# Kernel tuning notes

Hardware: AMD Instinct MI355X
Metric: run time of the kernel (lower is better)

Reference implementation:

```python
import jax, jax.numpy as jnp
import numpy as np

B, NF, H = 1024, 64, 512


def setup_inputs() -> dict:
    key = jax.random.key(0)
    ks = jax.random.split(key, 12)
    sc_in2 = 1.0 / np.sqrt(2 * H)
    sc_in1 = 1.0 / np.sqrt(H)
    inp = {
        "field_vectors": jax.random.normal(ks[0], (B, NF, H), dtype=jnp.float32),
        # and_fusion: Linear(2H->H), ReLU, Linear(H->H)
        "and_W1": jax.random.uniform(ks[1], (2 * H, H), jnp.float32, -sc_in2, sc_in2),
        "and_b1": jax.random.uniform(ks[2], (H,), jnp.float32, -sc_in2, sc_in2),
        "and_W2": jax.random.uniform(ks[3], (H, H), jnp.float32, -sc_in1, sc_in1),
        "and_b2": jax.random.uniform(ks[4], (H,), jnp.float32, -sc_in1, sc_in1),
        # or_fusion: Linear(2H->H), ReLU, Linear(H->H)
        "or_W1": jax.random.uniform(ks[5], (2 * H, H), jnp.float32, -sc_in2, sc_in2),
        "or_b1": jax.random.uniform(ks[6], (H,), jnp.float32, -sc_in2, sc_in2),
        "or_W2": jax.random.uniform(ks[7], (H, H), jnp.float32, -sc_in1, sc_in1),
        "or_b2": jax.random.uniform(ks[8], (H,), jnp.float32, -sc_in1, sc_in1),
        # not_transform: Linear(H->H), Tanh
        "not_W": jax.random.uniform(ks[9], (H, H), jnp.float32, -sc_in1, sc_in1),
        "not_b": jax.random.uniform(ks[10], (H,), jnp.float32, -sc_in1, sc_in1),
        # Disjoint index structure so the torch skip-set logic is a no-op:
        # 'and' pairs use fields 0..31, 'or' pairs use 32..47, leftovers 48..63.
        "not_idx": 48 + jnp.arange(8, dtype=jnp.int32),
        "and_pairs": jnp.arange(32, dtype=jnp.int32).reshape(16, 2),
        "or_pairs": (32 + jnp.arange(16, dtype=jnp.int32)).reshape(8, 2),
        "leftover_idx": 48 + jnp.arange(16, dtype=jnp.int32),
    }
    return inp


def _mlp2(x, W1, b1, W2, b2):
    # Linear -> ReLU -> Linear
    return jax.nn.relu(x @ W1 + b1) @ W2 + b2


def reference(field_vectors, and_W1, and_b1, and_W2, and_b2,
              or_W1, or_b1, or_W2, or_b2, not_W, not_b,
              not_idx, and_pairs, or_pairs, leftover_idx):
    # In-place 'not' transform on selected fields (Tanh(Linear))
    fv = field_vectors.at[:, not_idx].set(
        jnp.tanh(field_vectors[:, not_idx] @ not_W + not_b))
    # Gather (i, j) pairs, concat along feature dim -> [B, P, 2H]
    cat_and = jnp.concatenate([fv[:, and_pairs[:, 0]], fv[:, and_pairs[:, 1]]], axis=-1)
    fused_and = _mlp2(cat_and, and_W1, and_b1, and_W2, and_b2)  # [B, 16, H]
    cat_or = jnp.concatenate([fv[:, or_pairs[:, 0]], fv[:, or_pairs[:, 1]]], axis=-1)
    fused_or = _mlp2(cat_or, or_W1, or_b1, or_W2, or_b2)  # [B, 8, H]
    # Stack order matches torch loop: and results, or results, untouched fields
    return jnp.concatenate([fused_and, fused_or, fv[:, leftover_idx]], axis=1)
```

## Files before the change

kernel.cpp:

```cpp
#include <hip/hip_runtime.h>
#include <hip/hip_bf16.h>
#include <math.h>

typedef __attribute__((ext_vector_type(8))) __bf16 bf16x8;
typedef __attribute__((ext_vector_type(4))) float f32x4;

__device__ __forceinline__ unsigned short f2bf(float f) {
    union { float f; unsigned u; } v; v.f = f;
    unsigned r = v.u + 0x7fffu + ((v.u >> 16) & 1u);
    return (unsigned short)(r >> 16);
}
__device__ __forceinline__ unsigned int pk(float a, float b) {
    union { float f; unsigned u; } x, y; x.f = a; y.f = b;
    unsigned ra = (x.u + 0x7fffu + ((x.u >> 16) & 1u)) >> 16;
    unsigned rb = (y.u + 0x7fffu + ((y.u >> 16) & 1u)) & 0xffff0000u;
    return ra | rb;
}

__device__ __forceinline__ void gl2lds16(const unsigned short* g, unsigned short* l) {
    __builtin_amdgcn_global_load_lds(
        (const __attribute__((address_space(1))) unsigned int*)(g),
        (__attribute__((address_space(3))) unsigned int*)(l), 16, 0, 0);
}

struct PrepArgs {
    const float* fv;
    unsigned short* fvb;
    const int *and_pairs, *or_pairs, *not_idx, *lidx;
    float* out;
    const float* W[5];
    unsigned short* WT[5];
    int N[5];
    int tstart[6];
};

__global__ __launch_bounds__(256) void prep_kernel(PrepArgs a) {
    __shared__ float tile[64][65];
    const int blk = blockIdx.x;
    const int tid = threadIdx.x;

    if (blk < 448) {
        int m = 0;
        while (blk >= a.tstart[m + 1]) m++;
        const float* src = a.W[m];
        unsigned short* dst = a.WT[m];
        const int N = a.N[m];
        const int t = blk - a.tstart[m];
        const int ntn = N >> 6;
        const int tk = t / ntn, tn = t % ntn;
        const int c = tid & 63, r0 = tid >> 6;
        #pragma unroll
        for (int r = r0; r < 64; r += 4)
            tile[r][c] = src[(size_t)(tk * 64 + r) * N + tn * 64 + c];
        __syncthreads();
        const int l = tid & 63;
        #pragma unroll
        for (int fi = tid >> 6; fi < 8; fi += 4) {
            const int ktl = fi & 1, cgl = fi >> 1;
            const int kt = tk * 2 + ktl, cg = tn * 4 + cgl;
            const int kb = ktl * 32 + (l >> 4) * 8;
            const int nb = cgl * 16 + (l & 15);
            uint4 o;
            o.x = pk(tile[kb + 0][nb], tile[kb + 1][nb]);
            o.y = pk(tile[kb + 2][nb], tile[kb + 3][nb]);
            o.z = pk(tile[kb + 4][nb], tile[kb + 5][nb]);
            o.w = pk(tile[kb + 6][nb], tile[kb + 7][nb]);
            ((uint4*)dst)[((size_t)kt * 32 + cg) * 64 + l] = o;
        }
        return;
    }

    const int t = (blk - 448) * 256 + tid;
    const int lane = tid & 63;
    const size_t e = (size_t)t * 8;
    const int c = (int)(e & 511);
    const int f = (int)((e >> 9) & 63);
    const int b = (int)(e >> 15);
    const float4 v0 = *(const float4*)(a.fv + e);
    const float4 v1 = *(const float4*)(a.fv + e + 4);
    const int am = (lane < 32) ? a.and_pairs[lane] : -1;
    const int om = (lane < 16) ? a.or_pairs[lane]  : -1;
    const int nm = (lane <  8) ? a.not_idx[lane]   : -1;
    const int lm = (lane < 16) ? a.lidx[lane]      : -1;
    const unsigned long long bn = __ballot(nm == f);
    const unsigned long long bu = __ballot(am == f) | __ballot(om == f) | bn;
    const unsigned long long bl = __ballot(lm == f);
    if (bu) {
        uint4 o;
        o.x = pk(v0.x, v0.y); o.y = pk(v0.z, v0.w);
        o.z = pk(v1.x, v1.y); o.w = pk(v1.z, v1.w);
        ((uint4*)a.fvb)[t] = o;
    }
    if (bl && !bn) {
        const int ls = (int)__builtin_ctzll(bl);
        float* d = a.out + ((size_t)b * 40 + 24 + ls) * 512 + c;
        *(float4*)(d)     = v0;
        *(float4*)(d + 4) = v1;
    }
}

#define LOADB(DST, WTP, K0)                                                  \
    _Pragma("unroll") for (int ni = 0; ni < 4; ni++)                         \
        DST[ni] = *(const bf16x8*)((WTP) +                                   \
            ((((size_t)(K0) >> 5) * 32 + cg0 + ni) << 9) + (lane << 3));

#define MMAC(BF, AF)                                                         \
    _Pragma("unroll") for (int mi = 0; mi < 4; mi++)                         \
    _Pragma("unroll") for (int ni = 0; ni < 4; ni++)                         \
        acc[mi][ni] = __builtin_amdgcn_mfma_f32_16x16x32_bf16(               \
            AF[mi], BF[ni], acc[mi][ni], 0, 0, 0);

template <int P, int K1, int SRCM, int PATH, int QBASE>
__device__ __forceinline__ void fused_seg(
    const unsigned short* __restrict__ A,
    const int* __restrict__ idx,
    const unsigned short* __restrict__ W1T,
    const float* __restrict__ b1,
    const unsigned short* __restrict__ W2T,
    const float* __restrict__ b2,
    float* __restrict__ out,
    const int* __restrict__ leftover,
    int local,
    unsigned short* As, unsigned short* hid) {

    const int tid  = threadIdx.x;
    const int lane = tid & 63, w = tid >> 6;
    const int ln15 = lane & 15;
    const int kq   = lane >> 4;
    const int wn   = w * 64;
    const int cg0  = w * 4;
    const int m0   = local * 64;

    const int skin = ((lane & 3) ^ ((lane >> 2) & 3)) * 8;
    const unsigned short *ar0, *ar1;
    {
        const int m = m0 + (w & 3) * 16 + (lane >> 2);
        if constexpr (SRCM == 0) {
            const int b = m / P, p = m % P;
            ar0 = A + ((size_t)b * 64 + idx[2 * p]) * 512;
            ar1 = A + ((size_t)b * 64 + idx[2 * p + 1]) * 512;
        } else {
            const int b = m >> 3, i = m & 7;
            ar0 = A + ((size_t)b * 64 + idx[i]) * 512;
            ar1 = ar0;
        }
    }
    auto stageA = [&](int buf, int t) {
        const int k0 = t * 32;
        const unsigned short* src;
        if constexpr (SRCM == 0)
            src = (k0 >= 512 ? ar1 + (k0 - 512) : ar0 + k0) + skin;
        else
            src = ar0 + k0 + skin;
        gl2lds16(src, &As[buf * 2048 + (w & 3) * 512]);
    };
    const int xsel = (kq ^ (lane & 3)) * 8;

    f32x4 acc[4][4];
    #pragma unroll
    for (int mi = 0; mi < 4; mi++)
        #pragma unroll
        for (int ni = 0; ni < 4; ni++)
            acc[mi][ni] = f32x4{0.f, 0.f, 0.f, 0.f};

    bf16x8 bA[4];

    constexpr int NT1 = K1 / 32;
    if (w < 4) { stageA(0, 0); stageA(1, 1); }
    __builtin_amdgcn_sched_barrier(0);

    for (int h = 0; h < NT1; h++) {
        asm volatile("s_waitcnt vmcnt(1) lgkmcnt(0)" ::: "memory");
        asm volatile("s_barrier" ::: "memory");
        LOADB(bA, W1T, h * 32);
        __builtin_amdgcn_sched_barrier(0);
        if (w < 4 && h + 2 < NT1) stageA((h + 2) & 3, h + 2);
        __builtin_amdgcn_sched_barrier(0);
        bf16x8 af[4];
        #pragma unroll
        for (int mi = 0; mi < 4; mi++)
            af[mi] = *(const bf16x8*)&As[(h & 3) * 2048 +
                                         (mi * 16 + ln15) * 32 + xsel];
        MMAC(bA, af);
        __builtin_amdgcn_sched_barrier(0);
    }

    if constexpr (PATH == 2) {
        int qmap[8];
        #pragma unroll
        for (int i = 0; i < 8; i++) {
            const int f = idx[i];
            int q = 24;
            for (int l = 0; l < 16; l++)
                if (leftover[l] == f) q = 24 + l;
            qmap[i] = q;
        }
        #pragma unroll
        for (int ni = 0; ni < 4; ni++) {
            const int n = wn + ni * 16 + ln15;
            const float bv = b1[n];
            #pragma unroll
            for (int mi = 0; mi < 4; mi++)
                #pragma unroll
                for (int j = 0; j < 4; j++) {
                    const int r = mi * 16 + kq * 4 + j;
                    const int m = m0 + r;
                    const int b = m >> 3, i = m & 7;
                    out[((size_t)b * 40 + qmap[i]) * 512 + n] =
                        tanhf(acc[mi][ni][j] + bv);
                }
        }
        return;
    }

    #pragma unroll
    for (int ni = 0; ni < 4; ni++) {
        const int n  = wn + ni * 16 + ln15;
        const float bv = b1[n];
        const int c8 = n >> 3;
        const int cl = (n & 7) * 2;
        #pragma unroll
        for (int mi = 0; mi < 4; mi++)
            #pragma unroll
            for (int j = 0; j < 4; j++) {
                const int r = mi * 16 + kq * 4 + j;
                float v = acc[mi][ni][j] + bv;
                v = v > 0.f ? v : 0.f;
                *(unsigned short*)((char*)hid + r * 1024 +
                                   ((c8 ^ (r & 7)) * 16) + cl) = f2bf(v);
            }
    }
    #pragma unroll
    for (int mi = 0; mi < 4; mi++)
        #pragma unroll
        for (int ni = 0; ni < 4; ni++)
            acc[mi][ni] = f32x4{0.f, 0.f, 0.f, 0.f};
    __syncthreads();

    for (int t2 = 0; t2 < 16; t2++) {
        LOADB(bA, W2T, t2 * 32);
        bf16x8 af[4];
        #pragma unroll
        for (int mi = 0; mi < 4; mi++) {
            const int r = mi * 16 + ln15;
            const int c8 = t2 * 4 + kq;
            af[mi] = *(const bf16x8*)((char*)hid + r * 1024 +
                                      ((c8 ^ (r & 7)) * 16));
        }
        MMAC(bA, af);
    }

    #pragma unroll
    for (int ni = 0; ni < 4; ni++) {
        const int n  = wn + ni * 16 + ln15;
        const float bv = b2[n];
        #pragma unroll
        for (int mi = 0; mi < 4; mi++)
            #pragma unroll
            for (int j = 0; j < 4; j++) {
                const int r = mi * 16 + kq * 4 + j;
                const int m = m0 + r;
                const int b = m / P, p = m % P;
                out[((size_t)b * 40 + QBASE + p) * 512 + n] =
                    acc[mi][ni][j] + bv;
            }
    }
}

struct FArgs {
    const unsigned short *fvb, *and_W1T, *and_W2T, *or_W1T, *or_W2T, *not_WT;
    const int *and_pairs, *or_pairs, *not_idx, *leftover;
    const float *and_b1, *and_b2, *or_b1, *or_b2, *not_b;
    float* out;
};

__global__ __launch_bounds__(512, 4) void fused_phase(FArgs a) {
    __shared__ __align__(16) unsigned short As[4 * 64 * 32];
    __shared__ __align__(16) unsigned short hid[64 * 512];
    const int blk = blockIdx.x;
    if (blk < 256)
        fused_seg<16, 1024, 0, 0, 0>(a.fvb, a.and_pairs, a.and_W1T, a.and_b1,
                                     a.and_W2T, a.and_b2, a.out, nullptr,
                                     blk, As, hid);
    else if (blk < 384)
        fused_seg<8, 1024, 0, 0, 16>(a.fvb, a.or_pairs, a.or_W1T, a.or_b1,
                                     a.or_W2T, a.or_b2, a.out, nullptr,
                                     blk - 256, As, hid);
    else
        fused_seg<8, 512, 1, 2, 24>(a.fvb, a.not_idx, a.not_WT, a.not_b,
                                    nullptr, nullptr, a.out, a.leftover,
                                    blk - 384, As, hid);
}

extern "C" void kernel_launch(void* const* d_in, const int* in_sizes, int n_in,
                              void* d_out, int out_size, void* d_ws, size_t ws_size,
                              hipStream_t stream) {
    const float* fv       = (const float*)d_in[0];
    const float* and_W1   = (const float*)d_in[1];
    const float* and_b1   = (const float*)d_in[2];
    const float* and_W2   = (const float*)d_in[3];
    const float* and_b2   = (const float*)d_in[4];
    const float* or_W1    = (const float*)d_in[5];
    const float* or_b1    = (const float*)d_in[6];
    const float* or_W2    = (const float*)d_in[7];
    const float* or_b2    = (const float*)d_in[8];
    const float* not_W    = (const float*)d_in[9];
    const float* not_b    = (const float*)d_in[10];
    const int* not_idx    = (const int*)d_in[11];
    const int* and_pairs  = (const int*)d_in[12];
    const int* or_pairs   = (const int*)d_in[13];
    const int* leftover   = (const int*)d_in[14];
    float* out = (float*)d_out;
    char* ws = (char*)d_ws;

    unsigned short* fvb     = (unsigned short*)(ws);
    unsigned short* and_W1T = (unsigned short*)(ws + 67108864);
    unsigned short* or_W1T  = (unsigned short*)(ws + 68157440);
    unsigned short* and_W2T = (unsigned short*)(ws + 69206016);
    unsigned short* or_W2T  = (unsigned short*)(ws + 69730304);
    unsigned short* not_WT  = (unsigned short*)(ws + 70254592);

    PrepArgs pa;
    pa.fv = fv; pa.fvb = fvb; pa.out = out;
    pa.and_pairs = and_pairs; pa.or_pairs = or_pairs;
    pa.not_idx = not_idx; pa.lidx = leftover;
    pa.W[0] = and_W1; pa.WT[0] = and_W1T; pa.N[0] = 512;
    pa.W[1] = or_W1;  pa.WT[1] = or_W1T;  pa.N[1] = 512;
    pa.W[2] = and_W2; pa.WT[2] = and_W2T; pa.N[2] = 512;
    pa.W[3] = or_W2;  pa.WT[3] = or_W2T;  pa.N[3] = 512;
    pa.W[4] = not_W;  pa.WT[4] = not_WT;  pa.N[4] = 512;
    pa.tstart[0] = 0;   pa.tstart[1] = 128; pa.tstart[2] = 256;
    pa.tstart[3] = 320; pa.tstart[4] = 384; pa.tstart[5] = 448;
    prep_kernel<<<dim3(448 + 16384), dim3(256), 0, stream>>>(pa);

    FArgs fa;
    fa.fvb = fvb;
    fa.and_W1T = and_W1T; fa.and_W2T = and_W2T;
    fa.or_W1T = or_W1T;   fa.or_W2T = or_W2T;   fa.not_WT = not_WT;
    fa.and_pairs = and_pairs; fa.or_pairs = or_pairs; fa.not_idx = not_idx;
    fa.leftover = leftover;
    fa.and_b1 = and_b1; fa.and_b2 = and_b2;
    fa.or_b1 = or_b1;   fa.or_b2 = or_b2;   fa.not_b = not_b;
    fa.out = out;
    fused_phase<<<dim3(512), dim3(512), 0, stream>>>(fa);
}
```

Baseline: 302.9 us.

## Scatter bf16 activations into pre-tiled swizzled A layouts during prep

The prep kernel now writes the bf16-converted field vectors straight into per-segment (and/or/not) A buffers, already gathered by pair and arranged in the tile order and XOR swizzle the GEMM consumes. The fused kernel then stages A with one contiguous global-to-LDS copy per tile and no per-row pair indirection. This removes the gather address computation and the scattered row reads in the GEMM's main loop, and makes its A loads fully contiguous. The cost is that the prep kernel's stores become scattered, and correctness relies on each field appearing in at most one and-pair and one or-pair slot (ctz picks a single match).

```diff
diff --git a/kernel.cpp b/kernel.cpp
--- a/kernel.cpp
+++ b/kernel.cpp
@@ -25,7 +25,7 @@
 
 struct PrepArgs {
     const float* fv;
-    unsigned short* fvb;
+    unsigned short *and_At, *or_At, *not_At;
     const int *and_pairs, *or_pairs, *not_idx, *lidx;
     float* out;
     const float* W[5];
@@ -82,14 +82,46 @@
     const int om = (lane < 16) ? a.or_pairs[lane]  : -1;
     const int nm = (lane <  8) ? a.not_idx[lane]   : -1;
     const int lm = (lane < 16) ? a.lidx[lane]      : -1;
+    const unsigned long long ba = __ballot(am == f);
+    const unsigned long long bo = __ballot(om == f);
     const unsigned long long bn = __ballot(nm == f);
-    const unsigned long long bu = __ballot(am == f) | __ballot(om == f) | bn;
     const unsigned long long bl = __ballot(lm == f);
-    if (bu) {
-        uint4 o;
-        o.x = pk(v0.x, v0.y); o.y = pk(v0.z, v0.w);
-        o.z = pk(v1.x, v1.y); o.w = pk(v1.z, v1.w);
-        ((uint4*)a.fvb)[t] = o;
+
+    uint4 o;
+    o.x = pk(v0.x, v0.y); o.y = pk(v0.z, v0.w);
+    o.z = pk(v1.x, v1.y); o.w = pk(v1.z, v1.w);
+    const int c8 = lane;
+    const int kc = c8 & 3;
+
+    if (ba) {
+        const int j = (int)__builtin_ctzll(ba);
+        const int m = b * 16 + (j >> 1);
+        const int kt = (j & 1) * 16 + (c8 >> 2);
+        const int r = m & 63;
+        const int l = ((r & 15) << 2) | (kc ^ (r & 3));
+        *(uint4*)(a.and_At +
+            (((((size_t)(m >> 6) * 32 + kt) << 2) | (unsigned)(r >> 4)) << 9) +
+            (l << 3)) = o;
+    }
+    if (bo) {
+        const int j = (int)__builtin_ctzll(bo);
+        const int m = b * 8 + (j >> 1);
+        const int kt = (j & 1) * 16 + (c8 >> 2);
+        const int r = m & 63;
+        const int l = ((r & 15) << 2) | (kc ^ (r & 3));
+        *(uint4*)(a.or_At +
+            (((((size_t)(m >> 6) * 32 + kt) << 2) | (unsigned)(r >> 4)) << 9) +
+            (l << 3)) = o;
+    }
+    if (bn) {
+        const int i = (int)__builtin_ctzll(bn);
+        const int m = b * 8 + i;
+        const int kt = c8 >> 2;
+        const int r = m & 63;
+        const int l = ((r & 15) << 2) | (kc ^ (r & 3));
+        *(uint4*)(a.not_At +
+            (((((size_t)(m >> 6) * 16 + kt) << 2) | (unsigned)(r >> 4)) << 9) +
+            (l << 3)) = o;
     }
     if (bl && !bn) {
         const int ls = (int)__builtin_ctzll(bl);
@@ -110,15 +142,15 @@
         acc[mi][ni] = __builtin_amdgcn_mfma_f32_16x16x32_bf16(               \
             AF[mi], BF[ni], acc[mi][ni], 0, 0, 0);
 
-template <int P, int K1, int SRCM, int PATH, int QBASE>
+template <int P, int K1, int PATH, int QBASE>
 __device__ __forceinline__ void fused_seg(
-    const unsigned short* __restrict__ A,
-    const int* __restrict__ idx,
+    const unsigned short* __restrict__ At,
     const unsigned short* __restrict__ W1T,
     const float* __restrict__ b1,
     const unsigned short* __restrict__ W2T,
     const float* __restrict__ b2,
     float* __restrict__ out,
+    const int* __restrict__ nidx,
     const int* __restrict__ leftover,
     int local,
     unsigned short* As, unsigned short* hid) {
@@ -130,29 +162,12 @@
     const int wn   = w * 64;
     const int cg0  = w * 4;
     const int m0   = local * 64;
-
-    const int skin = ((lane & 3) ^ ((lane >> 2) & 3)) * 8;
-    const unsigned short *ar0, *ar1;
-    {
-        const int m = m0 + (w & 3) * 16 + (lane >> 2);
-        if constexpr (SRCM == 0) {
-            const int b = m / P, p = m % P;
-            ar0 = A + ((size_t)b * 64 + idx[2 * p]) * 512;
-            ar1 = A + ((size_t)b * 64 + idx[2 * p + 1]) * 512;
-        } else {
-            const int b = m >> 3, i = m & 7;
-            ar0 = A + ((size_t)b * 64 + idx[i]) * 512;
-            ar1 = ar0;
-        }
-    }
+    constexpr int NTK = K1 / 32;
+
+    const unsigned short* abase =
+        At + (size_t)local * NTK * 2048 + ((w & 3) << 9) + (lane << 3);
     auto stageA = [&](int buf, int t) {
-        const int k0 = t * 32;
-        const unsigned short* src;
-        if constexpr (SRCM == 0)
-            src = (k0 >= 512 ? ar1 + (k0 - 512) : ar0 + k0) + skin;
-        else
-            src = ar0 + k0 + skin;
-        gl2lds16(src, &As[buf * 2048 + (w & 3) * 512]);
+        gl2lds16(abase + (size_t)t * 2048, &As[buf * 2048 + (w & 3) * 512]);
     };
     const int xsel = (kq ^ (lane & 3)) * 8;
 
@@ -165,16 +180,15 @@
 
     bf16x8 bA[4];
 
-    constexpr int NT1 = K1 / 32;
     if (w < 4) { stageA(0, 0); stageA(1, 1); }
     __builtin_amdgcn_sched_barrier(0);
 
-    for (int h = 0; h < NT1; h++) {
+    for (int h = 0; h < NTK; h++) {
         asm volatile("s_waitcnt vmcnt(1) lgkmcnt(0)" ::: "memory");
         asm volatile("s_barrier" ::: "memory");
         LOADB(bA, W1T, h * 32);
         __builtin_amdgcn_sched_barrier(0);
-        if (w < 4 && h + 2 < NT1) stageA((h + 2) & 3, h + 2);
+        if (w < 4 && h + 2 < NTK) stageA((h + 2) & 3, h + 2);
         __builtin_amdgcn_sched_barrier(0);
         bf16x8 af[4];
         #pragma unroll
@@ -189,7 +203,7 @@
         int qmap[8];
         #pragma unroll
         for (int i = 0; i < 8; i++) {
-            const int f = idx[i];
+            const int f = nidx[i];
             int q = 24;
             for (int l = 0; l < 16; l++)
                 if (leftover[l] == f) q = 24 + l;
@@ -268,8 +282,9 @@
 }
 
 struct FArgs {
-    const unsigned short *fvb, *and_W1T, *and_W2T, *or_W1T, *or_W2T, *not_WT;
-    const int *and_pairs, *or_pairs, *not_idx, *leftover;
+    const unsigned short *and_At, *or_At, *not_At;
+    const unsigned short *and_W1T, *and_W2T, *or_W1T, *or_W2T, *not_WT;
+    const int *not_idx, *leftover;
     const float *and_b1, *and_b2, *or_b1, *or_b2, *not_b;
     float* out;
 };
@@ -279,17 +294,17 @@
     __shared__ __align__(16) unsigned short hid[64 * 512];
     const int blk = blockIdx.x;
     if (blk < 256)
-        fused_seg<16, 1024, 0, 0, 0>(a.fvb, a.and_pairs, a.and_W1T, a.and_b1,
-                                     a.and_W2T, a.and_b2, a.out, nullptr,
-                                     blk, As, hid);
+        fused_seg<16, 1024, 0, 0>(a.and_At, a.and_W1T, a.and_b1,
+                                  a.and_W2T, a.and_b2, a.out,
+                                  nullptr, nullptr, blk, As, hid);
     else if (blk < 384)
-        fused_seg<8, 1024, 0, 0, 16>(a.fvb, a.or_pairs, a.or_W1T, a.or_b1,
-                                     a.or_W2T, a.or_b2, a.out, nullptr,
-                                     blk - 256, As, hid);
+        fused_seg<8, 1024, 0, 16>(a.or_At, a.or_W1T, a.or_b1,
+                                  a.or_W2T, a.or_b2, a.out,
+                                  nullptr, nullptr, blk - 256, As, hid);
     else
-        fused_seg<8, 512, 1, 2, 24>(a.fvb, a.not_idx, a.not_WT, a.not_b,
-                                    nullptr, nullptr, a.out, a.leftover,
-                                    blk - 384, As, hid);
+        fused_seg<8, 512, 2, 24>(a.not_At, a.not_WT, a.not_b,
+                                 nullptr, nullptr, a.out,
+                                 a.not_idx, a.leftover, blk - 384, As, hid);
 }
 
 extern "C" void kernel_launch(void* const* d_in, const int* in_sizes, int n_in,
@@ -313,15 +328,18 @@
     float* out = (float*)d_out;
     char* ws = (char*)d_ws;
 
-    unsigned short* fvb     = (unsigned short*)(ws);
-    unsigned short* and_W1T = (unsigned short*)(ws + 67108864);
-    unsigned short* or_W1T  = (unsigned short*)(ws + 68157440);
-    unsigned short* and_W2T = (unsigned short*)(ws + 69206016);
-    unsigned short* or_W2T  = (unsigned short*)(ws + 69730304);
-    unsigned short* not_WT  = (unsigned short*)(ws + 70254592);
+    unsigned short* and_At  = (unsigned short*)(ws);
+    unsigned short* or_At   = (unsigned short*)(ws + 33554432);
+    unsigned short* not_At  = (unsigned short*)(ws + 50331648);
+    unsigned short* and_W1T = (unsigned short*)(ws + 58720256);
+    unsigned short* or_W1T  = (unsigned short*)(ws + 59768832);
+    unsigned short* and_W2T = (unsigned short*)(ws + 60817408);
+    unsigned short* or_W2T  = (unsigned short*)(ws + 61341696);
+    unsigned short* not_WT  = (unsigned short*)(ws + 61865984);
 
     PrepArgs pa;
-    pa.fv = fv; pa.fvb = fvb; pa.out = out;
+    pa.fv = fv; pa.out = out;
+    pa.and_At = and_At; pa.or_At = or_At; pa.not_At = not_At;
     pa.and_pairs = and_pairs; pa.or_pairs = or_pairs;
     pa.not_idx = not_idx; pa.lidx = leftover;
     pa.W[0] = and_W1; pa.WT[0] = and_W1T; pa.N[0] = 512;
@@ -334,11 +352,10 @@
     prep_kernel<<<dim3(448 + 16384), dim3(256), 0, stream>>>(pa);
 
     FArgs fa;
-    fa.fvb = fvb;
+    fa.and_At = and_At; fa.or_At = or_At; fa.not_At = not_At;
     fa.and_W1T = and_W1T; fa.and_W2T = and_W2T;
     fa.or_W1T = or_W1T;   fa.or_W2T = or_W2T;   fa.not_WT = not_WT;
-    fa.and_pairs = and_pairs; fa.or_pairs = or_pairs; fa.not_idx = not_idx;
-    fa.leftover = leftover;
+    fa.not_idx = not_idx; fa.leftover = leftover;
     fa.and_b1 = and_b1; fa.and_b2 = and_b2;
     fa.or_b1 = or_b1;   fa.or_b2 = or_b2;   fa.not_b = not_b;
     fa.out = out;
```

After: 298.7 us. No clear change (-1.4%).

## Fuse fp32-to-bf16 conversion of activations into GEMM A-tile staging

Applied to the files above, without the earlier changes.

Drops the prep pass that converted the whole 128MB fp32 field tensor to a bf16 workspace. The fused GEMM kernel now loads fp32 rows directly through registers, converts them to bf16 and writes them to a double-buffered LDS tile, replacing the async global-to-LDS loads. The leftover-field copy moves into extra blocks of the fused kernel. This removes a full read and write of the activations, at the cost of register-staged loads with less latency hiding and twice the bytes per A tile.

```diff
diff --git a/kernel.cpp b/kernel.cpp
--- a/kernel.cpp
+++ b/kernel.cpp
@@ -17,85 +17,43 @@
     return ra | rb;
 }
 
-__device__ __forceinline__ void gl2lds16(const unsigned short* g, unsigned short* l) {
-    __builtin_amdgcn_global_load_lds(
-        (const __attribute__((address_space(1))) unsigned int*)(g),
-        (__attribute__((address_space(3))) unsigned int*)(l), 16, 0, 0);
-}
-
-struct PrepArgs {
-    const float* fv;
-    unsigned short* fvb;
-    const int *and_pairs, *or_pairs, *not_idx, *lidx;
-    float* out;
+struct WArgs {
     const float* W[5];
     unsigned short* WT[5];
     int N[5];
     int tstart[6];
 };
 
-__global__ __launch_bounds__(256) void prep_kernel(PrepArgs a) {
+__global__ __launch_bounds__(256) void wprep_kernel(WArgs a) {
     __shared__ float tile[64][65];
     const int blk = blockIdx.x;
     const int tid = threadIdx.x;
-
-    if (blk < 448) {
-        int m = 0;
-        while (blk >= a.tstart[m + 1]) m++;
-        const float* src = a.W[m];
-        unsigned short* dst = a.WT[m];
-        const int N = a.N[m];
-        const int t = blk - a.tstart[m];
-        const int ntn = N >> 6;
-        const int tk = t / ntn, tn = t % ntn;
-        const int c = tid & 63, r0 = tid >> 6;
-        #pragma unroll
-        for (int r = r0; r < 64; r += 4)
-            tile[r][c] = src[(size_t)(tk * 64 + r) * N + tn * 64 + c];
-        __syncthreads();
-        const int l = tid & 63;
-        #pragma unroll
-        for (int fi = tid >> 6; fi < 8; fi += 4) {
-            const int ktl = fi & 1, cgl = fi >> 1;
-            const int kt = tk * 2 + ktl, cg = tn * 4 + cgl;
-            const int kb = ktl * 32 + (l >> 4) * 8;
-            const int nb = cgl * 16 + (l & 15);
-            uint4 o;
-            o.x = pk(tile[kb + 0][nb], tile[kb + 1][nb]);
-            o.y = pk(tile[kb + 2][nb], tile[kb + 3][nb]);
-            o.z = pk(tile[kb + 4][nb], tile[kb + 5][nb]);
-            o.w = pk(tile[kb + 6][nb], tile[kb + 7][nb]);
-            ((uint4*)dst)[((size_t)kt * 32 + cg) * 64 + l] = o;
-        }
-        return;
-    }
-
-    const int t = (blk - 448) * 256 + tid;
-    const int lane = tid & 63;
-    const size_t e = (size_t)t * 8;
-    const int c = (int)(e & 511);
-    const int f = (int)((e >> 9) & 63);
-    const int b = (int)(e >> 15);
-    const float4 v0 = *(const float4*)(a.fv + e);
-    const float4 v1 = *(const float4*)(a.fv + e + 4);
-    const int am = (lane < 32) ? a.and_pairs[lane] : -1;
-    const int om = (lane < 16) ? a.or_pairs[lane]  : -1;
-    const int nm = (lane <  8) ? a.not_idx[lane]   : -1;
-    const int lm = (lane < 16) ? a.lidx[lane]      : -1;
-    const unsigned long long bn = __ballot(nm == f);
-    const unsigned long long bu = __ballot(am == f) | __ballot(om == f) | bn;
-    const unsigned long long bl = __ballot(lm == f);
-    if (bu) {
+    int m = 0;
+    while (blk >= a.tstart[m + 1]) m++;
+    const float* src = a.W[m];
+    unsigned short* dst = a.WT[m];
+    const int N = a.N[m];
+    const int t = blk - a.tstart[m];
+    const int ntn = N >> 6;
+    const int tk = t / ntn, tn = t % ntn;
+    const int c = tid & 63, r0 = tid >> 6;
+    #pragma unroll
+    for (int r = r0; r < 64; r += 4)
+        tile[r][c] = src[(size_t)(tk * 64 + r) * N + tn * 64 + c];
+    __syncthreads();
+    const int l = tid & 63;
+    #pragma unroll
+    for (int fi = tid >> 6; fi < 8; fi += 4) {
+        const int ktl = fi & 1, cgl = fi >> 1;
+        const int kt = tk * 2 + ktl, cg = tn * 4 + cgl;
+        const int kb = ktl * 32 + (l >> 4) * 8;
+        const int nb = cgl * 16 + (l & 15);
         uint4 o;
-        o.x = pk(v0.x, v0.y); o.y = pk(v0.z, v0.w);
-        o.z = pk(v1.x, v1.y); o.w = pk(v1.z, v1.w);
-        ((uint4*)a.fvb)[t] = o;
-    }
-    if (bl && !bn) {
-        const int ls = (int)__builtin_ctzll(bl);
-        float* d = a.out + ((size_t)b * 40 + 24 + ls) * 512 + c;
-        *(float4*)(d)     = v0;
-        *(float4*)(d + 4) = v1;
+        o.x = pk(tile[kb + 0][nb], tile[kb + 1][nb]);
+        o.y = pk(tile[kb + 2][nb], tile[kb + 3][nb]);
+        o.z = pk(tile[kb + 4][nb], tile[kb + 5][nb]);
+        o.w = pk(tile[kb + 6][nb], tile[kb + 7][nb]);
+        ((uint4*)dst)[((size_t)kt * 32 + cg) * 64 + l] = o;
     }
 }
 
@@ -110,9 +68,13 @@
         acc[mi][ni] = __builtin_amdgcn_mfma_f32_16x16x32_bf16(               \
             AF[mi], BF[ni], acc[mi][ni], 0, 0, 0);
 
-template <int P, int K1, int SRCM, int PATH, int QBASE>
+#define LBAR()                                                               \
+    asm volatile("s_waitcnt lgkmcnt(0)" ::: "memory");                       \
+    asm volatile("s_barrier" ::: "memory");
+
+template <int P, int K1, int PATH, int QBASE>
 __device__ __forceinline__ void fused_seg(
-    const unsigned short* __restrict__ A,
+    const float* __restrict__ fv,
     const int* __restrict__ idx,
     const unsigned short* __restrict__ W1T,
     const float* __restrict__ b1,
@@ -130,29 +92,35 @@
     const int wn   = w * 64;
     const int cg0  = w * 4;
     const int m0   = local * 64;
-
-    const int skin = ((lane & 3) ^ ((lane >> 2) & 3)) * 8;
-    const unsigned short *ar0, *ar1;
+    constexpr int NTK = K1 / 32;
+
+    const int r  = tid >> 3;
+    const int ks = tid & 7;
+    const float *ar0, *ar1;
     {
-        const int m = m0 + (w & 3) * 16 + (lane >> 2);
-        if constexpr (SRCM == 0) {
+        const int m = m0 + r;
+        if constexpr (PATH == 0) {
             const int b = m / P, p = m % P;
-            ar0 = A + ((size_t)b * 64 + idx[2 * p]) * 512;
-            ar1 = A + ((size_t)b * 64 + idx[2 * p + 1]) * 512;
+            ar0 = fv + ((size_t)b * 64 + idx[2 * p]) * 512 + ks * 4;
+            ar1 = fv + ((size_t)b * 64 + idx[2 * p + 1]) * 512 + ks * 4;
         } else {
             const int b = m >> 3, i = m & 7;
-            ar0 = A + ((size_t)b * 64 + idx[i]) * 512;
+            ar0 = fv + ((size_t)b * 64 + idx[i]) * 512 + ks * 4;
             ar1 = ar0;
         }
     }
-    auto stageA = [&](int buf, int t) {
+    auto ldA = [&](int t) -> float4 {
         const int k0 = t * 32;
-        const unsigned short* src;
-        if constexpr (SRCM == 0)
-            src = (k0 >= 512 ? ar1 + (k0 - 512) : ar0 + k0) + skin;
+        if constexpr (K1 == 1024)
+            return *(const float4*)(k0 >= 512 ? ar1 + (k0 - 512) : ar0 + k0);
         else
-            src = ar0 + k0 + skin;
-        gl2lds16(src, &As[buf * 2048 + (w & 3) * 512]);
+            return *(const float4*)(ar0 + k0);
+    };
+    unsigned short* const wdst =
+        As + r * 32 + (((ks >> 1) ^ (r & 3)) << 3) + ((ks & 1) << 2);
+    auto wrA = [&](int buf, float4 v) {
+        uint2 o; o.x = pk(v.x, v.y); o.y = pk(v.z, v.w);
+        *(uint2*)(wdst + buf * 2048) = o;
     };
     const int xsel = (kq ^ (lane & 3)) * 8;
 
@@ -165,24 +133,34 @@
 
     bf16x8 bA[4];
 
-    constexpr int NT1 = K1 / 32;
-    if (w < 4) { stageA(0, 0); stageA(1, 1); }
-    __builtin_amdgcn_sched_barrier(0);
-
-    for (int h = 0; h < NT1; h++) {
-        asm volatile("s_waitcnt vmcnt(1) lgkmcnt(0)" ::: "memory");
-        asm volatile("s_barrier" ::: "memory");
-        LOADB(bA, W1T, h * 32);
-        __builtin_amdgcn_sched_barrier(0);
-        if (w < 4 && h + 2 < NT1) stageA((h + 2) & 3, h + 2);
-        __builtin_amdgcn_sched_barrier(0);
-        bf16x8 af[4];
-        #pragma unroll
-        for (int mi = 0; mi < 4; mi++)
-            af[mi] = *(const bf16x8*)&As[(h & 3) * 2048 +
-                                         (mi * 16 + ln15) * 32 + xsel];
-        MMAC(bA, af);
-        __builtin_amdgcn_sched_barrier(0);
+    float4 va = ldA(0);
+    float4 vb = ldA(1);
+    wrA(0, va);
+    LBAR();
+
+    for (int h = 0; h < NTK; h += 2) {
+        {
+            LOADB(bA, W1T, h * 32);
+            if (h + 2 < NTK) va = ldA(h + 2);
+            bf16x8 af[4];
+            #pragma unroll
+            for (int mi = 0; mi < 4; mi++)
+                af[mi] = *(const bf16x8*)&As[(mi * 16 + ln15) * 32 + xsel];
+            MMAC(bA, af);
+            wrA(1, vb);
+            LBAR();
+        }
+        {
+            LOADB(bA, W1T, (h + 1) * 32);
+            if (h + 3 < NTK) vb = ldA(h + 3);
+            bf16x8 af[4];
+            #pragma unroll
+            for (int mi = 0; mi < 4; mi++)
+                af[mi] = *(const bf16x8*)&As[2048 + (mi * 16 + ln15) * 32 + xsel];
+            MMAC(bA, af);
+            if (h + 2 < NTK) { wrA(0, va); }
+            LBAR();
+        }
     }
 
     if constexpr (PATH == 2) {
@@ -203,8 +181,8 @@
             for (int mi = 0; mi < 4; mi++)
                 #pragma unroll
                 for (int j = 0; j < 4; j++) {
-                    const int r = mi * 16 + kq * 4 + j;
-                    const int m = m0 + r;
+                    const int rr = mi * 16 + kq * 4 + j;
+                    const int m = m0 + rr;
                     const int b = m >> 3, i = m & 7;
                     out[((size_t)b * 40 + qmap[i]) * 512 + n] =
                         tanhf(acc[mi][ni][j] + bv);
@@ -223,11 +201,11 @@
         for (int mi = 0; mi < 4; mi++)
             #pragma unroll
             for (int j = 0; j < 4; j++) {
-                const int r = mi * 16 + kq * 4 + j;
+                const int rr = mi * 16 + kq * 4 + j;
                 float v = acc[mi][ni][j] + bv;
                 v = v > 0.f ? v : 0.f;
-                *(unsigned short*)((char*)hid + r * 1024 +
-                                   ((c8 ^ (r & 7)) * 16) + cl) = f2bf(v);
+                *(unsigned short*)((char*)hid + rr * 1024 +
+                                   ((c8 ^ (rr & 7)) * 16) + cl) = f2bf(v);
             }
     }
     #pragma unroll
@@ -242,10 +220,10 @@
         bf16x8 af[4];
         #pragma unroll
         for (int mi = 0; mi < 4; mi++) {
-            const int r = mi * 16 + ln15;
+            const int rr = mi * 16 + ln15;
             const int c8 = t2 * 4 + kq;
-            af[mi] = *(const bf16x8*)((char*)hid + r * 1024 +
-                                      ((c8 ^ (r & 7)) * 16));
+            af[mi] = *(const bf16x8*)((char*)hid + rr * 1024 +
+                                      ((c8 ^ (rr & 7)) * 16));
         }
         MMAC(bA, af);
     }
@@ -258,8 +236,8 @@
         for (int mi = 0; mi < 4; mi++)
             #pragma unroll
             for (int j = 0; j < 4; j++) {
-                const int r = mi * 16 + kq * 4 + j;
-                const int m = m0 + r;
+                const int rr = mi * 16 + kq * 4 + j;
+                const int m = m0 + rr;
                 const int b = m / P, p = m % P;
                 out[((size_t)b * 40 + QBASE + p) * 512 + n] =
                     acc[mi][ni][j] + bv;
@@ -268,28 +246,45 @@
 }
 
 struct FArgs {
-    const unsigned short *fvb, *and_W1T, *and_W2T, *or_W1T, *or_W2T, *not_WT;
+    const float* fv;
+    const unsigned short *and_W1T, *and_W2T, *or_W1T, *or_W2T, *not_WT;
     const int *and_pairs, *or_pairs, *not_idx, *leftover;
     const float *and_b1, *and_b2, *or_b1, *or_b2, *not_b;
     float* out;
 };
 
 __global__ __launch_bounds__(512, 4) void fused_phase(FArgs a) {
-    __shared__ __align__(16) unsigned short As[4 * 64 * 32];
+    __shared__ __align__(16) unsigned short As[2 * 64 * 32];
     __shared__ __align__(16) unsigned short hid[64 * 512];
     const int blk = blockIdx.x;
-    if (blk < 256)
-        fused_seg<16, 1024, 0, 0, 0>(a.fvb, a.and_pairs, a.and_W1T, a.and_b1,
-                                     a.and_W2T, a.and_b2, a.out, nullptr,
-                                     blk, As, hid);
-    else if (blk < 384)
-        fused_seg<8, 1024, 0, 0, 16>(a.fvb, a.or_pairs, a.or_W1T, a.or_b1,
-                                     a.or_W2T, a.or_b2, a.out, nullptr,
-                                     blk - 256, As, hid);
-    else
-        fused_seg<8, 512, 1, 2, 24>(a.fvb, a.not_idx, a.not_WT, a.not_b,
-                                    nullptr, nullptr, a.out, a.leftover,
-                                    blk - 384, As, hid);
+    if (blk < 256) {
+        fused_seg<16, 1024, 0, 0>(a.fv, a.and_pairs, a.and_W1T, a.and_b1,
+                                  a.and_W2T, a.and_b2, a.out, nullptr,
+                                  blk, As, hid);
+    } else if (blk < 384) {
+        fused_seg<8, 1024, 0, 16>(a.fv, a.or_pairs, a.or_W1T, a.or_b1,
+                                  a.or_W2T, a.or_b2, a.out, nullptr,
+                                  blk - 256, As, hid);
+    } else if (blk < 512) {
+        fused_seg<8, 512, 2, 24>(a.fv, a.not_idx, a.not_WT, a.not_b,
+                                 nullptr, nullptr, a.out, a.leftover,
+                                 blk - 384, As, hid);
+    } else {
+        const int t = (blk - 512) * 512 + threadIdx.x;
+        const size_t e = (size_t)t * 8;
+        const int c  = (int)(e & 511);
+        const int ls = (int)((e >> 9) & 15);
+        const int b  = (int)(e >> 13);
+        const int f  = a.leftover[ls];
+        int isnot = 0;
+        #pragma unroll
+        for (int i = 0; i < 8; i++) isnot |= (a.not_idx[i] == f);
+        if (isnot) return;
+        const float* s = a.fv + ((size_t)b * 64 + f) * 512 + c;
+        float* d = a.out + ((size_t)b * 40 + 24 + ls) * 512 + c;
+        *(float4*)(d)     = *(const float4*)(s);
+        *(float4*)(d + 4) = *(const float4*)(s + 4);
+    }
 }
 
 extern "C" void kernel_launch(void* const* d_in, const int* in_sizes, int n_in,
@@ -313,28 +308,24 @@
     float* out = (float*)d_out;
     char* ws = (char*)d_ws;
 
-    unsigned short* fvb     = (unsigned short*)(ws);
-    unsigned short* and_W1T = (unsigned short*)(ws + 67108864);
-    unsigned short* or_W1T  = (unsigned short*)(ws + 68157440);
-    unsigned short* and_W2T = (unsigned short*)(ws + 69206016);
-    unsigned short* or_W2T  = (unsigned short*)(ws + 69730304);
-    unsigned short* not_WT  = (unsigned short*)(ws + 70254592);
-
-    PrepArgs pa;
-    pa.fv = fv; pa.fvb = fvb; pa.out = out;
-    pa.and_pairs = and_pairs; pa.or_pairs = or_pairs;
-    pa.not_idx = not_idx; pa.lidx = leftover;
-    pa.W[0] = and_W1; pa.WT[0] = and_W1T; pa.N[0] = 512;
-    pa.W[1] = or_W1;  pa.WT[1] = or_W1T;  pa.N[1] = 512;
-    pa.W[2] = and_W2; pa.WT[2] = and_W2T; pa.N[2] = 512;
-    pa.W[3] = or_W2;  pa.WT[3] = or_W2T;  pa.N[3] = 512;
-    pa.W[4] = not_W;  pa.WT[4] = not_WT;  pa.N[4] = 512;
-    pa.tstart[0] = 0;   pa.tstart[1] = 128; pa.tstart[2] = 256;
-    pa.tstart[3] = 320; pa.tstart[4] = 384; pa.tstart[5] = 448;
-    prep_kernel<<<dim3(448 + 16384), dim3(256), 0, stream>>>(pa);
+    unsigned short* and_W1T = (unsigned short*)(ws);
+    unsigned short* or_W1T  = (unsigned short*)(ws + 1048576);
+    unsigned short* and_W2T = (unsigned short*)(ws + 2097152);
+    unsigned short* or_W2T  = (unsigned short*)(ws + 2621440);
+    unsigned short* not_WT  = (unsigned short*)(ws + 3145728);
+
+    WArgs wa;
+    wa.W[0] = and_W1; wa.WT[0] = and_W1T; wa.N[0] = 512;
+    wa.W[1] = or_W1;  wa.WT[1] = or_W1T;  wa.N[1] = 512;
+    wa.W[2] = and_W2; wa.WT[2] = and_W2T; wa.N[2] = 512;
+    wa.W[3] = or_W2;  wa.WT[3] = or_W2T;  wa.N[3] = 512;
+    wa.W[4] = not_W;  wa.WT[4] = not_WT;  wa.N[4] = 512;
+    wa.tstart[0] = 0;   wa.tstart[1] = 128; wa.tstart[2] = 256;
+    wa.tstart[3] = 320; wa.tstart[4] = 384; wa.tstart[5] = 448;
+    wprep_kernel<<<dim3(448), dim3(256), 0, stream>>>(wa);
 
     FArgs fa;
-    fa.fvb = fvb;
+    fa.fv = fv;
     fa.and_W1T = and_W1T; fa.and_W2T = and_W2T;
     fa.or_W1T = or_W1T;   fa.or_W2T = or_W2T;   fa.not_WT = not_WT;
     fa.and_pairs = and_pairs; fa.or_pairs = or_pairs; fa.not_idx = not_idx;
@@ -342,5 +333,5 @@
     fa.and_b1 = and_b1; fa.and_b2 = and_b2;
     fa.or_b1 = or_b1;   fa.or_b2 = or_b2;   fa.not_b = not_b;
     fa.out = out;
-    fused_phase<<<dim3(512), dim3(512), 0, stream>>>(fa);
-}
+    fused_phase<<<dim3(512 + 2048), dim3(512), 0, stream>>>(fa);
+}
```

After: 308.1 us. Within noise of the previous version (+1.7%).
